# Kernel optimization log

Measured on AMD Instinct MI355X. Metric: run time of the kernel, lower is better.

## Reference

```python
import jax, jax.numpy as jnp
import numpy as np
from jax import lax

EPS = 1e-07
PATCH = 3  # patch_size -> padding = 1 with 1x1 kernels
PROP = 3   # propagate_size -> 3x3 sum pool (avg_pool*9)


def setup_inputs() -> dict:
    key = jax.random.key(0)
    k1, k2 = jax.random.split(key)
    foreground = jax.random.normal(k1, (4, 128, 64, 64), dtype=jnp.float32)
    mask = jax.random.uniform(k2, (4, 1, 64, 64), dtype=jnp.float32)
    return {"foreground": foreground, "mask": mask}


def _cattention_single(x, m):
    # x: (c, h, w); m: (1, h, w)
    c, h, w = x.shape
    pad = PATCH // 2  # = 1
    # dynamic 1x1 conv kernels: (h*w, c), one kernel per spatial location
    k = x.reshape(c, h * w).T + EPS
    k = k / jnp.sqrt(jnp.sum(k * k, axis=1, keepdims=True))
    # F.conv2d(x, k, padding=1) with 1x1 kernels -> zero-pad then matmul
    x_pad = jnp.pad(x, ((0, 0), (pad, pad), (pad, pad)))  # (c, h+2, w+2)
    scores = jnp.einsum('lc,cij->lij', k, x_pad)  # (hw, h+2, w+2)
    # avg_pool2d(3,1,padding=1) * 9 == 3x3 sum pool with zero padding
    scores = lax.reduce_window(scores, 0.0, lax.add,
                               window_dimensions=(1, 3, 3),
                               window_strides=(1, 1, 1),
                               padding=((0, 0), (1, 1), (1, 1)))
    att = jax.nn.softmax(scores, axis=0)  # softmax over the hw channel dim
    # conv_transpose2d with 1x1 kernels, padding=1 -> crop border then matmul
    att_c = att[:, pad:-pad, pad:-pad]  # (hw, h, w)
    recovered = jnp.einsum('lij,lc->cij', att_c, k)  # (c, h, w)
    recovered = recovered * (1.0 - m) / float(PATCH ** 2)
    return recovered + x * m


def reference(foreground, mask):
    return jax.vmap(_cattention_single)(foreground, mask)
```

## Files before the change

kernel.cpp:

```cpp
#include <hip/hip_runtime.h>


typedef short bf16x8 __attribute__((ext_vector_type(8)));
typedef float f32x4 __attribute__((ext_vector_type(4)));
typedef unsigned int u32x2 __attribute__((ext_vector_type(2)));

#define L2E 1.4426950408889634f

__device__ __forceinline__ unsigned short f2bf(float f) {
    unsigned int u;
    __builtin_memcpy(&u, &f, 4);
    u = u + 0x7FFFu + ((u >> 16) & 1u);
    return (unsigned short)(u >> 16);
}
__device__ __forceinline__ unsigned int pk_bf16(float a, float b) {
    unsigned int ua, ub;
    __builtin_memcpy(&ua, &a, 4);
    __builtin_memcpy(&ub, &b, 4);
    return ((ua + 0x8000u) >> 16) | ((ub + 0x8000u) & 0xFFFF0000u);
}

__global__ void prep_inv(const float* __restrict__ x, float* __restrict__ inv) {
    const int b = blockIdx.y, l = blockIdx.x * 256 + threadIdx.x;
    const float* xb = x + (size_t)b * 128 * 4096 + l;
    float sq = 0.f;
#pragma unroll 16
    for (int c = 0; c < 128; c++) {
        float v = xb[(size_t)c * 4096] + 1e-7f;
        sq += v * v;
    }
    inv[b * 4096 + l] = rsqrtf(sq);
}

__global__ void prep_main(const float* __restrict__ x,
                          const float* __restrict__ inv,
                          unsigned short* __restrict__ kmat,
                          unsigned short* __restrict__ kT,
                          unsigned short* __restrict__ xbT) {
    const int p = blockIdx.x, b = blockIdx.y, cb = blockIdx.z * 64;
    const int t = threadIdx.x, wave = t >> 6, lane = t & 63;

    __shared__ float sX[8][3][66];
    __shared__ float sMidT[64 * 68];
    __shared__ __align__(16) unsigned short sQ[64 * 80];
    __shared__ float sInv[64];
    if (t < 64) sInv[t] = inv[b * 4096 + p * 64 + t];

    for (int c0 = 0; c0 < 64; c0 += 8) {
        __syncthreads();
#pragma unroll
        for (int i = 0; i < 6; i++) {
            int pair = wave * 6 + i;
            int cc = pair / 3, r = pair - cc * 3;
            int pp = p + r - 1;
            float v = 0.f;
            if ((unsigned)pp < 64u)
                v = x[((size_t)b * 128 + cb + c0 + cc) * 4096 + pp * 64 + lane];
            sX[cc][r][1 + lane] = v;
        }
        if (t < 48) {
            int cc = t / 6, rr = (t % 6) >> 1, side = t & 1;
            sX[cc][rr][side * 65] = 0.f;
        }
        __syncthreads();
#pragma unroll
        for (int j = 0; j < 2; j++) {
            int cc = wave * 2 + j;
            float mid = sX[cc][1][1 + lane] + 1e-7f;
            sMidT[lane * 68 + c0 + cc] = mid;
            float sbox = 0.f;
#pragma unroll
            for (int r = 0; r < 3; r++)
                sbox += sX[cc][r][lane] + sX[cc][r][lane + 1] + sX[cc][r][lane + 2];
            sQ[lane * 80 + c0 + cc] = f2bf(sbox * L2E);
        }
    }
    __syncthreads();

#pragma unroll
    for (int i = 0; i < 2; i++) {
        int u = i * 256 + t, row = u >> 3, g = u & 7;
        *(bf16x8*)(xbT + ((size_t)b * 4096 + p * 64 + row) * 128 + cb + g * 8) =
            *(const bf16x8*)(sQ + row * 80 + g * 8);
    }
#pragma unroll
    for (int i = 0; i < 2; i++) {
        int u = i * 256 + t, q = u >> 3, g = u & 7;
        float iv = sInv[q];
        f32x4 a = *(const f32x4*)(sMidT + q * 68 + g * 8);
        f32x4 c = *(const f32x4*)(sMidT + q * 68 + g * 8 + 4);
        unsigned int w[4];
        w[0] = pk_bf16(a[0] * iv, a[1] * iv);
        w[1] = pk_bf16(a[2] * iv, a[3] * iv);
        w[2] = pk_bf16(c[0] * iv, c[1] * iv);
        w[3] = pk_bf16(c[2] * iv, c[3] * iv);
        *(uint4*)(kmat + ((size_t)b * 4096 + p * 64 + q) * 128 + cb + g * 8) =
            make_uint4(w[0], w[1], w[2], w[3]);
    }
    {
        int c = t >> 2, qg = t & 3;
        unsigned int w[8];
#pragma unroll
        for (int j = 0; j < 8; j++) {
            int ql = qg * 16 + j * 2;
            w[j] = pk_bf16(sMidT[ql * 68 + c] * sInv[ql],
                           sMidT[(ql + 1) * 68 + c] * sInv[ql + 1]);
        }
        unsigned short* dst = kT + ((size_t)b * 128 + cb + c) * 4096 + p * 64 + qg * 16;
        *(uint4*)(dst) = make_uint4(w[0], w[1], w[2], w[3]);
        *(uint4*)(dst + 8) = make_uint4(w[4], w[5], w[6], w[7]);
    }
}

#define SK_STRIDE 136
#define SV_STRIDE 72
#define SP_STRIDE 72
#define SK_ELEMS (64 * SK_STRIDE)
#define SV_ELEMS (128 * SV_STRIDE)
#define SP_ELEMS (4 * 32 * SP_STRIDE)

__global__ void __launch_bounds__(256, 2) flash_attn(
        const unsigned short* __restrict__ kmat,
        const unsigned short* __restrict__ kT,
        const unsigned short* __restrict__ xbT,
        float* __restrict__ opart,
        float* __restrict__ lsum,
        int nsplit, int qbshift) {
    const int combo = blockIdx.x & (4 * nsplit - 1);
    const int qb = blockIdx.x >> qbshift;
    const int b = combo & 3, split = combo >> 2;
    const int nk = 4096 / nsplit, NIT = nk >> 6, kt_base = split * nk;
    const int t = threadIdx.x;
    const int wave = t >> 6, lane = t & 63;
    const int l16 = lane & 15, quad = lane >> 4;

    __shared__ __align__(16) unsigned short smem[SK_ELEMS + SV_ELEMS + SP_ELEMS];
    unsigned short* sK = smem;
    unsigned short* sV = smem + SK_ELEMS;
    unsigned short* sP = smem + SK_ELEMS + SV_ELEMS + wave * 32 * SP_STRIDE;

    bf16x8 aq[2][4];
#pragma unroll
    for (int h = 0; h < 2; h++) {
        const unsigned short* xq =
            xbT + ((size_t)b * 4096 + qb * 128 + wave * 32 + h * 16 + l16) * 128 + quad * 8;
#pragma unroll
        for (int cc = 0; cc < 4; cc++) aq[h][cc] = *(const bf16x8*)(xq + cc * 32);
    }

    f32x4 o[2][8];
#pragma unroll
    for (int h = 0; h < 2; h++)
#pragma unroll
        for (int n = 0; n < 8; n++) o[h][n] = (f32x4){0.f, 0.f, 0.f, 0.f};
    float rs[2] = {0.f, 0.f};

    const unsigned short* kmb = kmat + (size_t)b * 4096 * 128;
    const unsigned short* ktb = kT + (size_t)b * 128 * 4096;

    bf16x8 kreg[4], vreg[4];
#pragma unroll
    for (int i = 0; i < 4; i++) {
        int e = i * 2048 + t * 8;
        kreg[i] = *(const bf16x8*)(kmb + (size_t)(kt_base + (e >> 7)) * 128 + (e & 127));
        vreg[i] = *(const bf16x8*)(ktb + (size_t)(e >> 6) * 4096 + kt_base + (e & 63));
    }

    for (int it = 0; it < NIT; it++) {
        __syncthreads();
#pragma unroll
        for (int i = 0; i < 4; i++) {
            int e = i * 2048 + t * 8;
            *(bf16x8*)(sK + (e >> 7) * SK_STRIDE + (e & 127)) = kreg[i];
            *(bf16x8*)(sV + (e >> 6) * SV_STRIDE + (e & 63)) = vreg[i];
        }
        __syncthreads();
        if (it + 1 < NIT) {
            int kt0 = kt_base + (it + 1) * 64;
#pragma unroll
            for (int i = 0; i < 4; i++) {
                int e = i * 2048 + t * 8;
                kreg[i] = *(const bf16x8*)(kmb + (size_t)(kt0 + (e >> 7)) * 128 + (e & 127));
                vreg[i] = *(const bf16x8*)(ktb + (size_t)(e >> 6) * 4096 + kt0 + (e & 63));
            }
        }

        f32x4 s[2][4];
#pragma unroll
        for (int h = 0; h < 2; h++)
#pragma unroll
            for (int k4 = 0; k4 < 4; k4++) s[h][k4] = (f32x4){0.f, 0.f, 0.f, 0.f};
#pragma unroll
        for (int cc = 0; cc < 4; cc++) {
#pragma unroll
            for (int k4 = 0; k4 < 4; k4++) {
                bf16x8 ak = *(const bf16x8*)(sK + (k4 * 16 + l16) * SK_STRIDE + cc * 32 + quad * 8);
                s[0][k4] = __builtin_amdgcn_mfma_f32_16x16x32_bf16(ak, aq[0][cc], s[0][k4], 0, 0, 0);
                s[1][k4] = __builtin_amdgcn_mfma_f32_16x16x32_bf16(ak, aq[1][cc], s[1][k4], 0, 0, 0);
            }
        }

#pragma unroll
        for (int h = 0; h < 2; h++) {
#pragma unroll
            for (int k4 = 0; k4 < 4; k4++) {
                float p0 = exp2f(s[h][k4][0]), p1 = exp2f(s[h][k4][1]);
                float p2 = exp2f(s[h][k4][2]), p3 = exp2f(s[h][k4][3]);
                rs[h] += (p0 + p1) + (p2 + p3);
                u32x2 d;
                d[0] = pk_bf16(p0, p1);
                d[1] = pk_bf16(p2, p3);
                *(u32x2*)(sP + (h * 16 + l16) * SP_STRIDE + k4 * 16 + quad * 4) = d;
            }
        }
        asm volatile("" ::: "memory");
        bf16x8 pa[2][2];
#pragma unroll
        for (int h = 0; h < 2; h++)
#pragma unroll
            for (int kc = 0; kc < 2; kc++)
                pa[h][kc] = *(const bf16x8*)(sP + (h * 16 + l16) * SP_STRIDE + kc * 32 + quad * 8);
        asm volatile("" ::: "memory");

#pragma unroll
        for (int kc = 0; kc < 2; kc++)
#pragma unroll
            for (int n = 0; n < 8; n++) {
                bf16x8 bv = *(const bf16x8*)(sV + (n * 16 + l16) * SV_STRIDE + kc * 32 + quad * 8);
                o[0][n] = __builtin_amdgcn_mfma_f32_16x16x32_bf16(pa[0][kc], bv, o[0][n], 0, 0, 0);
                o[1][n] = __builtin_amdgcn_mfma_f32_16x16x32_bf16(pa[1][kc], bv, o[1][n], 0, 0, 0);
            }
    }

#pragma unroll
    for (int h = 0; h < 2; h++) {
        rs[h] += __shfl_xor(rs[h], 16);
        rs[h] += __shfl_xor(rs[h], 32);
    }
    if (lane < 16) {
#pragma unroll
        for (int h = 0; h < 2; h++)
            lsum[(size_t)(split * 4 + b) * 4096 + qb * 128 + wave * 32 + h * 16 + lane] = rs[h];
    }

    float* sO = reinterpret_cast<float*>(smem);
#pragma unroll
    for (int half = 0; half < 2; half++) {
        __syncthreads();
        if ((wave >> 1) == half) {
#pragma unroll
            for (int h = 0; h < 2; h++)
#pragma unroll
                for (int n = 0; n < 8; n++)
#pragma unroll
                    for (int r = 0; r < 4; r++)
                        sO[(n * 16 + l16) * 68 + (wave & 1) * 32 + h * 16 + quad * 4 + r] =
                            o[h][n][r];
        }
        __syncthreads();
#pragma unroll
        for (int i = 0; i < 8; i++) {
            int c = (t >> 4) + i * 16, qj = (t & 15) * 4;
            *(f32x4*)(opart + ((size_t)(split * 4 + b) * 128 + c) * 4096 +
                      qb * 128 + half * 64 + qj) = *(const f32x4*)(sO + c * 68 + qj);
        }
    }
}

__global__ void combine(const float* __restrict__ opart,
                        const float* __restrict__ lsum,
                        const float* __restrict__ x,
                        const float* __restrict__ mask,
                        float* __restrict__ out, int S) {
    const int qb = blockIdx.x, b = blockIdx.y, t = threadIdx.x;
    __shared__ float Linv[64];
    if (t < 64) {
        float L = 0.f;
        for (int s2 = 0; s2 < S; s2++)
            L += lsum[(size_t)(s2 * 4 + b) * 4096 + qb * 64 + t];
        Linv[t] = 1.f / fmaxf(L, 1e-37f);
    }
    __syncthreads();
#pragma unroll
    for (int i = 0; i < 8; i++) {
        int c = (t >> 4) + i * 16, qj = (t & 15) * 4;
        size_t qoff = (size_t)qb * 64 + qj;
        f32x4 acc = (f32x4){0.f, 0.f, 0.f, 0.f};
        for (int s2 = 0; s2 < S; s2++) {
            f32x4 p = *(const f32x4*)(opart + ((size_t)(s2 * 4 + b) * 128 + c) * 4096 + qoff);
#pragma unroll
            for (int j = 0; j < 4; j++) acc[j] += p[j];
        }
        f32x4 xv = *(const f32x4*)(x + ((size_t)b * 128 + c) * 4096 + qoff);
        f32x4 mv = *(const f32x4*)(mask + (size_t)b * 4096 + qoff);
        f32x4 res;
#pragma unroll
        for (int j = 0; j < 4; j++)
            res[j] = acc[j] * Linv[qj + j] * (1.f - mv[j]) * (1.f / 9.f) + xv[j] * mv[j];
        *(f32x4*)(out + ((size_t)b * 128 + c) * 4096 + qoff) = res;
    }
}

extern "C" void kernel_launch(void* const* d_in, const int* in_sizes, int n_in,
                              void* d_out, int out_size, void* d_ws, size_t ws_size,
                              hipStream_t stream) {
    const float* x = (const float*)d_in[0];
    const float* mask = (const float*)d_in[1];
    float* out = (float*)d_out;
    char* ws = (char*)d_ws;
    unsigned short* kmat = (unsigned short*)(ws);
    unsigned short* kT   = (unsigned short*)(ws + (size_t)4 * 1024 * 1024);
    unsigned short* xbT  = (unsigned short*)(ws + (size_t)8 * 1024 * 1024);
    float* lsum          = (float*)(ws + (size_t)12 * 1024 * 1024);
    float* inv           = (float*)(ws + (size_t)12 * 1024 * 1024 + 256 * 1024);
    float* opart         = (float*)(ws + (size_t)12 * 1024 * 1024 + 512 * 1024);

    int S, qbshift;
    if (ws_size >= (size_t)46137344)      { S = 4; qbshift = 4; }
    else if (ws_size >= (size_t)29360128) { S = 2; qbshift = 3; }
    else if (ws_size >= (size_t)22020096) { S = 1; qbshift = 2; }
    else return;

    prep_inv<<<dim3(16, 4), 256, 0, stream>>>(x, inv);
    prep_main<<<dim3(64, 4, 2), 256, 0, stream>>>(x, inv, kmat, kT, xbT);
    flash_attn<<<dim3(32 * 4 * S), 256, 0, stream>>>(kmat, kT, xbT, opart, lsum, S, qbshift);
    combine<<<dim3(64, 4), 256, 0, stream>>>(opart, lsum, x, mask, out, S);
}
```

Before: 152.5 us.

## Alias P buffer into K smem, store bf16 partials, double split count

The per-wave P staging buffer now shares the K tile region in shared memory, guarded by an added barrier after the QK MFMAs. This shrinks LDS per block so the launch bound can ask for 4 blocks per CU. Partial outputs are written as bf16 instead of fp32, halving opart traffic, and the key-split count doubles to add parallelism. The costs are an extra per-iteration __syncthreads, lower precision in the partial sums, and more partials for combine to read.

```diff
diff --git a/kernel.cpp b/kernel.cpp
--- a/kernel.cpp
+++ b/kernel.cpp
@@ -3,6 +3,7 @@
 
 typedef short bf16x8 __attribute__((ext_vector_type(8)));
 typedef float f32x4 __attribute__((ext_vector_type(4)));
+typedef unsigned short u16x4 __attribute__((ext_vector_type(4)));
 typedef unsigned int u32x2 __attribute__((ext_vector_type(2)));
 
 #define L2E 1.4426950408889634f
@@ -12,6 +13,12 @@
     __builtin_memcpy(&u, &f, 4);
     u = u + 0x7FFFu + ((u >> 16) & 1u);
     return (unsigned short)(u >> 16);
+}
+__device__ __forceinline__ float bf2f(unsigned short h) {
+    unsigned int u = ((unsigned int)h) << 16;
+    float f;
+    __builtin_memcpy(&f, &u, 4);
+    return f;
 }
 __device__ __forceinline__ unsigned int pk_bf16(float a, float b) {
     unsigned int ua, ub;
@@ -115,15 +122,15 @@
 #define SK_STRIDE 136
 #define SV_STRIDE 72
 #define SP_STRIDE 72
-#define SK_ELEMS (64 * SK_STRIDE)
+#define SK_REGION 9216
 #define SV_ELEMS (128 * SV_STRIDE)
-#define SP_ELEMS (4 * 32 * SP_STRIDE)
-
-__global__ void __launch_bounds__(256, 2) flash_attn(
+#define SMEM_ELEMS (SK_REGION + SV_ELEMS)
+
+__global__ void __launch_bounds__(256, 4) flash_attn(
         const unsigned short* __restrict__ kmat,
         const unsigned short* __restrict__ kT,
         const unsigned short* __restrict__ xbT,
-        float* __restrict__ opart,
+        unsigned short* __restrict__ opart,
         float* __restrict__ lsum,
         int nsplit, int qbshift) {
     const int combo = blockIdx.x & (4 * nsplit - 1);
@@ -134,10 +141,10 @@
     const int wave = t >> 6, lane = t & 63;
     const int l16 = lane & 15, quad = lane >> 4;
 
-    __shared__ __align__(16) unsigned short smem[SK_ELEMS + SV_ELEMS + SP_ELEMS];
+    __shared__ __align__(16) unsigned short smem[SMEM_ELEMS];
     unsigned short* sK = smem;
-    unsigned short* sV = smem + SK_ELEMS;
-    unsigned short* sP = smem + SK_ELEMS + SV_ELEMS + wave * 32 * SP_STRIDE;
+    unsigned short* sV = smem + SK_REGION;
+    unsigned short* sP = smem + wave * 32 * SP_STRIDE;
 
     bf16x8 aq[2][4];
 #pragma unroll
@@ -199,6 +206,7 @@
                 s[1][k4] = __builtin_amdgcn_mfma_f32_16x16x32_bf16(ak, aq[1][cc], s[1][k4], 0, 0, 0);
             }
         }
+        __syncthreads();
 
 #pragma unroll
         for (int h = 0; h < 2; h++) {
@@ -243,31 +251,28 @@
             lsum[(size_t)(split * 4 + b) * 4096 + qb * 128 + wave * 32 + h * 16 + lane] = rs[h];
     }
 
-    float* sO = reinterpret_cast<float*>(smem);
-#pragma unroll
-    for (int half = 0; half < 2; half++) {
-        __syncthreads();
-        if ((wave >> 1) == half) {
-#pragma unroll
-            for (int h = 0; h < 2; h++)
-#pragma unroll
-                for (int n = 0; n < 8; n++)
-#pragma unroll
-                    for (int r = 0; r < 4; r++)
-                        sO[(n * 16 + l16) * 68 + (wave & 1) * 32 + h * 16 + quad * 4 + r] =
-                            o[h][n][r];
-        }
-        __syncthreads();
-#pragma unroll
-        for (int i = 0; i < 8; i++) {
-            int c = (t >> 4) + i * 16, qj = (t & 15) * 4;
-            *(f32x4*)(opart + ((size_t)(split * 4 + b) * 128 + c) * 4096 +
-                      qb * 128 + half * 64 + qj) = *(const f32x4*)(sO + c * 68 + qj);
-        }
-    }
-}
-
-__global__ void combine(const float* __restrict__ opart,
+    __syncthreads();
+    unsigned short* sO = smem;
+    unsigned int* sO32 = (unsigned int*)smem;
+#pragma unroll
+    for (int h = 0; h < 2; h++)
+#pragma unroll
+        for (int n = 0; n < 8; n++) {
+            int c = n * 16 + l16;
+            int q = wave * 32 + h * 16 + quad * 4;
+            sO32[(c * 144 + q) >> 1] = pk_bf16(o[h][n][0], o[h][n][1]);
+            sO32[(c * 144 + q + 2) >> 1] = pk_bf16(o[h][n][2], o[h][n][3]);
+        }
+    __syncthreads();
+#pragma unroll
+    for (int i = 0; i < 8; i++) {
+        int u = i * 256 + t, c = u >> 4, chunk = u & 15;
+        *(uint4*)(opart + ((size_t)(split * 4 + b) * 128 + c) * 4096 + qb * 128 + chunk * 8) =
+            *(const uint4*)(sO + c * 144 + chunk * 8);
+    }
+}
+
+__global__ void combine(const unsigned short* __restrict__ opart,
                         const float* __restrict__ lsum,
                         const float* __restrict__ x,
                         const float* __restrict__ mask,
@@ -287,9 +292,9 @@
         size_t qoff = (size_t)qb * 64 + qj;
         f32x4 acc = (f32x4){0.f, 0.f, 0.f, 0.f};
         for (int s2 = 0; s2 < S; s2++) {
-            f32x4 p = *(const f32x4*)(opart + ((size_t)(s2 * 4 + b) * 128 + c) * 4096 + qoff);
-#pragma unroll
-            for (int j = 0; j < 4; j++) acc[j] += p[j];
+            u16x4 pv = *(const u16x4*)(opart + ((size_t)(s2 * 4 + b) * 128 + c) * 4096 + qoff);
+#pragma unroll
+            for (int j = 0; j < 4; j++) acc[j] += bf2f(pv[j]);
         }
         f32x4 xv = *(const f32x4*)(x + ((size_t)b * 128 + c) * 4096 + qoff);
         f32x4 mv = *(const f32x4*)(mask + (size_t)b * 4096 + qoff);
@@ -312,13 +317,13 @@
     unsigned short* kT   = (unsigned short*)(ws + (size_t)4 * 1024 * 1024);
     unsigned short* xbT  = (unsigned short*)(ws + (size_t)8 * 1024 * 1024);
     float* lsum          = (float*)(ws + (size_t)12 * 1024 * 1024);
-    float* inv           = (float*)(ws + (size_t)12 * 1024 * 1024 + 256 * 1024);
-    float* opart         = (float*)(ws + (size_t)12 * 1024 * 1024 + 512 * 1024);
+    float* inv           = (float*)(ws + (size_t)12 * 1024 * 1024 + 512 * 1024);
+    unsigned short* opart = (unsigned short*)(ws + (size_t)13 * 1024 * 1024);
 
     int S, qbshift;
-    if (ws_size >= (size_t)46137344)      { S = 4; qbshift = 4; }
-    else if (ws_size >= (size_t)29360128) { S = 2; qbshift = 3; }
-    else if (ws_size >= (size_t)22020096) { S = 1; qbshift = 2; }
+    if (ws_size >= (size_t)45 * 1024 * 1024)      { S = 8; qbshift = 5; }
+    else if (ws_size >= (size_t)29 * 1024 * 1024) { S = 4; qbshift = 4; }
+    else if (ws_size >= (size_t)21 * 1024 * 1024) { S = 2; qbshift = 3; }
     else return;
 
     prep_inv<<<dim3(16, 4), 256, 0, stream>>>(x, inv);
```

After: 319.1 us. +109.2%, slower.
